# Performance work log

Measured on AMD Instinct MI355X. Metric: run time of the kernel, lower is better.

Reference implementation:

```python
import jax, jax.numpy as jnp
import numpy as np

N_USERS = 100000
N_LOCAS = 50000
N = N_USERS + N_LOCAS
D = 128   # embedding_dynamic_size
K = 128   # kg entity dim
S = 128   # static dim
NK = 50000  # kg rows
E = 2048  # number of events
LN_EPS = 1e-5
NORM_EPS = 1e-12


def setup_inputs() -> dict:
    key = jax.random.key(0)
    ks = jax.random.split(key, 24)
    f = jnp.float32
    rin = D + K + 1
    s_rnn = 1.0 / np.sqrt(D)
    s_pred = 1.0 / np.sqrt(2 * S + 2 * D + K)
    inp = {
        'embedding': jax.random.normal(ks[0], (N, D), f),
        'static': jax.random.normal(ks[1], (N, S), f),
        'kg': jax.random.normal(ks[2], (NK, K), f),
        'W_ih_u': jax.random.normal(ks[3], (D, rin), f) * s_rnn,
        'b_ih_u': jax.random.normal(ks[4], (D,), f) * s_rnn,
        'W_hh_u': jax.random.normal(ks[5], (D, D), f) * s_rnn,
        'b_hh_u': jax.random.normal(ks[6], (D,), f) * s_rnn,
        'W_ih_l': jax.random.normal(ks[7], (D, rin), f) * s_rnn,
        'b_ih_l': jax.random.normal(ks[8], (D,), f) * s_rnn,
        'W_hh_l': jax.random.normal(ks[9], (D, D), f) * s_rnn,
        'b_hh_l': jax.random.normal(ks[10], (D,), f) * s_rnn,
        'w_proj': jax.random.normal(ks[11], (D,), f),   # NormalLinear(1, D) weight, std=1/sqrt(1)=1
        'b_proj': jax.random.normal(ks[12], (D,), f),
        'ln_g': jnp.ones((D + K,), f),
        'ln_b': jnp.zeros((D + K,), f),
        'W_pred': jax.random.normal(ks[13], (S + D, 2 * S + 2 * D + K), f) * s_pred,
        'b_pred': jnp.zeros((S + D,), f),
        'delta_u': jax.random.uniform(ks[14], (E,), f),
        'delta_l': jax.random.uniform(ks[15], (E,), f),
        'idx_user': jax.random.randint(ks[16], (E,), 0, N_USERS, jnp.int32),
        'idx_loca': jax.random.randint(ks[17], (E,), 0, N_LOCAS, jnp.int32),
        'idx_prev': jax.random.randint(ks[18], (E,), 0, N_LOCAS, jnp.int32),
        'idx_know': jax.random.randint(ks[19], (E,), 0, NK, jnp.int32),
        'num_users': N_USERS,
    }
    return inp


def reference(embedding, static, kg, W_ih_u, b_ih_u, W_hh_u, b_hh_u,
              W_ih_l, b_ih_l, W_hh_l, b_hh_l, w_proj, b_proj, ln_g, ln_b,
              W_pred, b_pred, delta_u, delta_l,
              idx_user, idx_loca, idx_prev, idx_know, num_users):
    sg = jax.lax.stop_gradient

    def l2n(x):  # F.normalize along the feature dim (row vector)
        return x / jnp.maximum(jnp.linalg.norm(x), NORM_EPS)

    # event index preprocessing (matches idx_loca + num_users etc.)
    xs = (idx_user, idx_loca + num_users, idx_prev + num_users, idx_know,
          delta_u, delta_l)

    def step(carry, ev):
        emb, loss = carry
        iu, il, ip, ik, du, dl = ev
        u = emb[iu]        # [D]
        l = emb[il]        # [D]
        p = emb[ip]        # [D]
        kgr = kg[ik]       # [K]
        # projection: u * (1 + Linear(1->D)(delta_u))
        proj = u * (1.0 + w_proj * du + b_proj)
        # layer_norm over concat([emb_prev, kg_row]) of size D+K
        x = jnp.concatenate([p, kgr])
        mu = x.mean()
        var = jnp.mean((x - mu) ** 2)
        ln = (x - mu) / jnp.sqrt(var + LN_EPS) * ln_g + ln_b
        meta = jnp.concatenate([proj, ln, static[ip], static[iu]])  # [2S+2D+K]
        pred = W_pred @ meta + b_pred                               # [S+D]
        tgt = jnp.concatenate([l, static[il]])
        loss_pred = jnp.mean((pred - sg(tgt)) ** 2)
        # RNNCell updates (tanh), then L2-normalize
        x_u = jnp.concatenate([l, kgr, du[None]])
        new_u = l2n(jnp.tanh(W_ih_u @ x_u + b_ih_u + W_hh_u @ u + b_hh_u))
        x_l = jnp.concatenate([u, kgr, dl[None]])
        new_l = l2n(jnp.tanh(W_ih_l @ x_l + b_ih_l + W_hh_l @ l + b_hh_l))
        loss = loss + loss_pred \
                    + jnp.mean((new_u - sg(u)) ** 2) \
                    + jnp.mean((new_l - sg(l)) ** 2)
        emb = emb.at[iu].set(new_u).at[il].set(new_l)
        return (emb, loss), None

    (emb, loss), _ = jax.lax.scan(
        step, (embedding, jnp.asarray(0.0, embedding.dtype)), xs)
    return emb, loss
```

## Files before the change

### kernel.cpp

```cpp
#include <hip/hip_runtime.h>

#define DEVINL static __device__ __forceinline__

typedef float f32x4 __attribute__((ext_vector_type(4)));

constexpr int NUSER = 100000;
constexpr int D     = 128;
constexpr int METAN = 640;
constexpr int NT    = 256;
constexpr int CH    = 4;
constexpr int KP4   = 160;
constexpr int KR4   = 96;
constexpr int NCPY  = 1024;
constexpr int STW   = 640;

struct Params {
  const float *emb_in, *stat, *kg;
  const float *Wihu, *bihu, *Whhu, *bhhu;
  const float *Wihl, *bihl, *Whhl, *bhhl;
  const float *wproj, *bproj, *lng, *lnb, *Wpred, *bpred;
  const float *deltau, *deltal;
  const int *idxu, *idxl, *idxp, *idxk;
  float *emb;
  float *loss_slot;
  float *WpredT;
  float *WrnnT;
  float *brnn;
  float *wcol;
  float *loss_ev;
  float *stash;
  int *cnt_u, *cnt_w, *cnt_t;
  int *flag_u, *flag_l;
  int *done;
  int E, N, NLOC, NWORK;
};

DEVINL float loadx(const float* p) {
  return __hip_atomic_load(p, __ATOMIC_RELAXED, __HIP_MEMORY_SCOPE_AGENT);
}
DEVINL void storex(float* p, float v) {
  __hip_atomic_store(p, v, __ATOMIC_RELAXED, __HIP_MEMORY_SCOPE_AGENT);
}
DEVINL int loadcnt(const int* p) {
  return __hip_atomic_load(p, __ATOMIC_RELAXED, __HIP_MEMORY_SCOPE_AGENT);
}
DEVINL void storei(int* p, int v) {
  __hip_atomic_store(p, v, __ATOMIC_RELAXED, __HIP_MEMORY_SCOPE_AGENT);
}
DEVINL void sigadd(int* pp) {
  __hip_atomic_fetch_add(pp, 1, __ATOMIC_RELAXED, __HIP_MEMORY_SCOPE_AGENT);
}
DEVINL float dot4(float4 a, float4 b) { return a.x*b.x + a.y*b.y + a.z*b.z + a.w*b.w; }

DEVINL float4 block_sum4(float4 v, float4* s4) {
  #pragma unroll
  for (int o = 32; o; o >>= 1) {
    v.x += __shfl_xor(v.x, o, 64); v.y += __shfl_xor(v.y, o, 64);
    v.z += __shfl_xor(v.z, o, 64); v.w += __shfl_xor(v.w, o, 64);
  }
  if ((threadIdx.x & 63) == 0) s4[threadIdx.x >> 6] = v;
  __syncthreads();
  float4 r;
  r.x = s4[0].x + s4[1].x + s4[2].x + s4[3].x;
  r.y = s4[0].y + s4[1].y + s4[2].y + s4[3].y;
  r.z = s4[0].z + s4[1].z + s4[2].z + s4[3].z;
  r.w = s4[0].w + s4[1].w + s4[2].w + s4[3].w;
  __syncthreads();
  return r;
}

// ... 24 lines not shown
    float4 v = *(const float4*)(p.Wpred + (size_t)j * METAN + k4 * 4);
    ((float4*)p.WpredT)[k4 * 256 + j] = v;
  }
  for (int idx = tid; idx < 256 * KR4; idx += stride) {
    int j = idx / KR4, k4 = idx - j * KR4;
    int i = j & 127;
    const float* Wih = (j < 128) ? p.Wihu : p.Wihl;
    const float* Whh = (j < 128) ? p.Whhu : p.Whhl;
    float4 v; float* vp = (float*)&v;
    #pragma unroll
    for (int e = 0; e < 4; ++e) {
      int k = k4 * 4 + e;
      vp[e] = (k < 256) ? Wih[(size_t)i * 257 + k] : Whh[(size_t)i * 128 + (k - 256)];
    }
    ((float4*)p.WrnnT)[k4 * 256 + j] = v;
  }
  for (int j = tid; j < 256; j += stride) {
    int i = j & 127;
    p.brnn[j] = (j < 128) ? p.bihu[i] + p.bhhu[i] : p.bihl[i] + p.bhhl[i];
    p.wcol[j] = (j < 128) ? p.Wihu[(size_t)i * 257 + 256] : p.Wihl[(size_t)i * 257 + 256];
  }
}

__global__ __launch_bounds__(NT, 2) void k_main(Params p) {
  __shared__ __align__(16) float s_meta[CH][METAN];
  __shared__ __align__(16) float s_u[CH][D], s_l[CH][D], s_p[CH][D], s_kg[CH][D], s_sil[CH][D];
  __shared__ float4 s_r4[4];
  __shared__ unsigned long long s_redu[4][CH];
  __shared__ int s_ev[8][CH];
  __shared__ float s_dd[2][CH];

  const int tid = threadIdx.x, w = tid >> 6, lane = tid & 63;
  const int bid = blockIdx.x;

  if (bid >= p.NWORK && bid < p.NWORK + NCPY) {
    size_t gid = (size_t)(bid - p.NWORK) * NT + tid;
    size_t gs  = (size_t)NCPY * NT;
    size_t n4  = (size_t)p.N * 32;
    const f32x4* src = (const f32x4*)p.emb_in;
    f32x4* dst = (f32x4*)p.emb;
    size_t g = gid;
    for (; g + 3 * gs < n4; g += 4 * gs) {
      size_t g0 = g, g1 = g + gs, g2 = g + 2 * gs, g3 = g + 3 * gs;
      int r0 = (int)(g0 >> 5), r1 = (int)(g1 >> 5), r2 = (int)(g2 >> 5), r3 = (int)(g3 >> 5);
      int f0 = (r0 < NUSER) ? p.flag_u[r0] : p.flag_l[r0 - NUSER];
      int f1 = (r1 < NUSER) ? p.flag_u[r1] : p.flag_l[r1 - NUSER];
      int f2 = (r2 < NUSER) ? p.flag_u[r2] : p.flag_l[r2 - NUSER];
      int f3 = (r3 < NUSER) ? p.flag_u[r3] : p.flag_l[r3 - NUSER];
      f32x4 v0 = src[g0], v1 = src[g1], v2 = src[g2], v3 = src[g3];
      if (!f0) dst[g0] = v0;
      if (!f1) dst[g1] = v1;
      if (!f2) dst[g2] = v2;
      if (!f3) dst[g3] = v3;
    }
    for (; g < n4; g += gs) {
      int r = (int)(g >> 5);
      int f = (r < NUSER) ? p.flag_u[r] : p.flag_l[r - NUSER];
      f32x4 v = src[g];
      if (!f) dst[g] = v;
    }
    return;
  }

  const bool is_chain = (bid < p.NWORK);
  const int c = is_chain ? bid : bid - p.NWORK - NCPY;
  const int base = c * CH;
  const int nev = min(CH, p.E - base);
  if (nev <= 0) return;

  int iu_[CH], il_[CH], ip_[CH], ik_[CH];
  #pragma unroll
  for (int e = 0; e < CH; ++e) {
    int t = base + e; bool v = e < nev;
    iu_[e] = v ? p.idxu[t] : -1;
    il_[e] = v ? p.idxl[t] : -1;
    ip_[e] = v ? p.idxp[t] : -1;
    ik_[e] = v ? p.idxk[t] : 0;
  }

  if (is_chain) {
    float du_[CH], dl_[CH];
    #pragma unroll
    for (int e = 0; e < CH; ++e) {
      int t = base + e; bool v = e < nev;
      du_[e] = v ? p.deltau[t] : 0.f;
      dl_[e] = v ? p.deltal[t] : 0.f;
    }

    unsigned long long pk[CH] = {0ull,0ull,0ull,0ull};
    for (int s = tid; s < base; s += NT) {
      int ius = p.idxu[s], ils = p.idxl[s], ips = p.idxp[s];
      #pragma unroll
      for (int e = 0; e < CH; ++e) {
        unsigned long long a  = (ius == iu_[e]);
        unsigned long long wl = (ils == il_[e]);
        unsigned long long b  = (unsigned long long)((ils == il_[e]) + (ips == il_[e]));
        unsigned long long cc = (ils == ip_[e]);
        pk[e] += a | (wl << 16) | (b << 32) | (cc << 48);
      }
    }
    #pragma unroll
    for (int o = 32; o; o >>= 1) {
      #pragma unroll
      for (int e = 0; e < CH; ++e) pk[e] += __shfl_xor(pk[e], o, 64);
    }
    if (lane == 0) {
      #pragma unroll
      for (int e = 0; e < CH; ++e) s_redu[w][e] = pk[e];
    }
    __syncthreads();
    #pragma unroll
    for (int e = 0; e < CH; ++e)
      pk[e] = s_redu[0][e] + s_redu[1][e] + s_redu[2][e] + s_redu[3][e];
    __syncthreads();

    int A_[CH], WL_[CH], B_[CH], C_[CH];
    #pragma unroll
    for (int e = 0; e < CH; ++e) {
      int a  = (int)(pk[e] & 0xffff),        wl = (int)((pk[e] >> 16) & 0xffff);
      int b  = (int)((pk[e] >> 32) & 0xffff), cc = (int)((pk[e] >> 48) & 0xffff);
      #pragma unroll
      for (int s2 = 0; s2 < CH; ++s2) if (s2 < e) {
        a  += (iu_[s2] == iu_[e]);
        wl += (il_[s2] == il_[e]);
        b  += (il_[s2] == il_[e]) + (ip_[s2] == il_[e]);
        cc += (il_[s2] == ip_[e]);
      }
      A_[e] = a; WL_[e] = wl; B_[e] = b; C_[e] = cc;
    }
    bool internal = false;
    #pragma unroll
    for (int t2 = 1; t2 < CH; ++t2) if (t2 < nev) {
      #pragma unroll
      for (int s2 = 0; s2 < t2; ++s2)
        internal |= (iu_[s2] == iu_[t2]) | (il_[s2] == il_[t2]) |
                    (il_[s2] == ip_[t2]) | (ip_[s2] == il_[t2]);
    }

    if (tid == 0) {
      #pragma unroll
      for (int e = 0; e < CH; ++e) {
        s_ev[0][e] = iu_[e]; s_ev[1][e] = il_[e]; s_ev[2][e] = ip_[e];
        s_ev[3][e] = A_[e];  s_ev[4][e] = WL_[e]; s_ev[5][e] = B_[e];
        s_ev[6][e] = C_[e];  s_ev[7][e] = ik_[e];
        s_dd[0][e] = du_[e]; s_dd[1][e] = dl_[e];
      }
    }
    __syncthreads();

    auto PRELOAD = [&](int b0, int b1) {
      int e = w;
      if (e >= b0 && e < b1) {
        int iu = s_ev[0][e], ilr = s_ev[1][e] + NUSER, ipr = s_ev[2][e] + NUSER;
        int A = s_ev[3][e], WL = s_ev[4][e], Ck = s_ev[6][e], ik = s_ev[7][e];
        if (lane < 32) {
          int li = lane * 4;
          *(float4*)&s_kg[e][li] = *(const float4*)(p.kg + (size_t)ik * D + li);
        }
        int i0 = lane * 2;
        if (!A)  *(float2*)&s_u[e][i0] = *(const float2*)(p.emb_in + (size_t)iu  * D + i0);
        if (!WL) *(float2*)&s_l[e][i0] = *(const float2*)(p.emb_in + (size_t)ilr * D + i0);
        if (!Ck) *(float2*)&s_p[e][i0] = *(const float2*)(p.emb_in + (size_t)ipr * D + i0);
      }
    };

    auto SPIN = [&](int b0, int b1) {
      if (w == 0) {
        int e = b0 + lane;
        bool act = lane < (b1 - b0);
        int iu = 0, il = 0, ip = 0, A = 0, Bc = 0, Cc = 0;
        if (act) {
          iu = s_ev[0][e]; il = s_ev[1][e]; ip = s_ev[2][e];
          A = s_ev[3][e]; Bc = s_ev[5][e]; Cc = s_ev[6][e];
        }
        int guard = 0;
        while (true) {
          int x = loadcnt(&p.cnt_u[iu]);
          int y = loadcnt(&p.cnt_t[il]);
          int z = loadcnt(&p.cnt_w[ip]);
          bool ok = (!act) | ((x >= A) & (y >= Bc) & (z >= Cc));
          if (__all(ok)) break;
          if (++guard > (1 << 22)) break;
          __builtin_amdgcn_s_sleep(1);
        }
      }
      __syncthreads();
    };

    auto POSTLOAD = [&](int b0, int b1) {
      int e = w;
      if (e >= b0 && e < b1) {
        int iu = s_ev[0][e], ilr = s_ev[1][e] + NUSER, ipr = s_ev[2][e] + NUSER;
        int A = s_ev[3][e], WL = s_ev[4][e], Ck = s_ev[6][e];
        int i0 = lane * 2;
        if (A) {
          s_u[e][i0]   = loadx(p.emb + (size_t)iu * D + i0);
          s_u[e][i0+1] = loadx(p.emb + (size_t)iu * D + i0 + 1);
        }
        if (WL) {
          s_l[e][i0]   = loadx(p.emb + (size_t)ilr * D + i0);
          s_l[e][i0+1] = loadx(p.emb + (size_t)ilr * D + i0 + 1);
        }
        if (Ck) {
          s_p[e][i0]   = loadx(p.emb + (size_t)ipr * D + i0);
          s_p[e][i0+1] = loadx(p.emb + (size_t)ipr * D + i0 + 1);
        }
      }
    };

    auto RNNPROC = [&](int b0, int b1) {
      __syncthreads();
      const bool uc = (tid < 128);
      const float4* xo0 = (const float4*)(uc ? s_l[0] : s_u[0]);
      const float4* xo1 = (const float4*)(uc ? s_l[1] : s_u[1]);
      const float4* xo2 = (const float4*)(uc ? s_l[2] : s_u[2]);
      const float4* xo3 = (const float4*)(uc ? s_l[3] : s_u[3]);
      const float4* xk0 = (const float4*)s_kg[0];
      const float4* xk1 = (const float4*)s_kg[1];
      const float4* xk2 = (const float4*)s_kg[2];
      const float4* xk3 = (const float4*)s_kg[3];
      const float4* xs0 = (const float4*)(uc ? s_u[0] : s_l[0]);
      const float4* xs1 = (const float4*)(uc ? s_u[1] : s_l[1]);
      const float4* xs2 = (const float4*)(uc ? s_u[2] : s_l[2]);
      const float4* xs3 = (const float4*)(uc ? s_u[3] : s_l[3]);
      float ra0 = 0.f, ra1 = 0.f, ra2 = 0.f, ra3 = 0.f;
      const float4* wr = (const float4*)p.WrnnT + tid;
      #pragma unroll 8
      for (int k4 = 0; k4 < 32; ++k4) {
        float4 wv = wr[k4 * 256];
        ra0 += dot4(wv, xo0[k4]); ra1 += dot4(wv, xo1[k4]);
        ra2 += dot4(wv, xo2[k4]); ra3 += dot4(wv, xo3[k4]);
      }
      #pragma unroll 8
      for (int k4 = 32; k4 < 64; ++k4) {
        float4 wv = wr[k4 * 256];
        ra0 += dot4(wv, xk0[k4-32]); ra1 += dot4(wv, xk1[k4-32]);
        ra2 += dot4(wv, xk2[k4-32]); ra3 += dot4(wv, xk3[k4-32]);
      }
      #pragma unroll 8
      for (int k4 = 64; k4 < 96; ++k4) {
        float4 wv = wr[k4 * 256];
        ra0 += dot4(wv, xs0[k4-64]); ra1 += dot4(wv, xs1[k4-64]);
        ra2 += dot4(wv, xs2[k4-64]); ra3 += dot4(wv, xs3[k4-64]);
      }
      float brn = p.brnn[tid], wcv = p.wcol[tid];
      float d0 = uc ? s_dd[0][0] : s_dd[1][0];
      float d1 = uc ? s_dd[0][1] : s_dd[1][1];
      float d2 = uc ? s_dd[0][2] : s_dd[1][2];
      float d3 = uc ? s_dd[0][3] : s_dd[1][3];
      float h0 = tanhf(ra0 + brn + wcv * d0), h1 = tanhf(ra1 + brn + wcv * d1);
      float h2v = tanhf(ra2 + brn + wcv * d2), h3 = tanhf(ra3 + brn + wcv * d3);

      float4 SU, SL;
      half_sum4(make_float4(h0*h0, h1*h1, h2v*h2v, h3*h3), s_r4, &SU, &SL);
      float s0 = uc ? SU.x : SL.x, s1 = uc ? SU.y : SL.y;
      float s2 = uc ? SU.z : SL.z, s3 = uc ? SU.w : SL.w;
      float n0 = h0 / fmaxf(sqrtf(s0), 1e-12f), n1 = h1 / fmaxf(sqrtf(s1), 1e-12f);
      float n2 = h2v / fmaxf(sqrtf(s2), 1e-12f), n3 = h3 / fmaxf(sqrtf(s3), 1e-12f);

      float nv[CH] = {n0, n1, n2, n3};
      #pragma unroll
      for (int e = 0; e < CH; ++e) if (e >= b0 && e < b1) {
        if (tid < 128) storex(p.emb + (size_t)s_ev[0][e] * D + tid, nv[e]);
        else           storex(p.emb + ((size_t)s_ev[1][e] + NUSER) * D + (tid - 128), nv[e]);
      }
      __syncthreads();

      if (tid >= b0 && tid < b1) {
        __builtin_amdgcn_fence(__ATOMIC_RELEASE, "agent");
        sigadd(&p.cnt_u[s_ev[0][tid]]);
        sigadd(&p.cnt_t[s_ev[1][tid]]);
        sigadd(&p.cnt_w[s_ev[1][tid]]);
        sigadd(&p.cnt_t[s_ev[2][tid]]);
      }

      #pragma unroll
      for (int e = 0; e < CH; ++e) if (e >= b0 && e < b1) {
        float* st = p.stash + (size_t)(base + e) * STW;
        if (tid < 128) {
          storex(st + tid,       s_u[e][tid]);
          storex(st + 256 + tid, s_p[e][tid]);
          storex(st + 384 + tid, nv[e]);
        } else {
          int i = tid - 128;
          storex(st + 128 + i, s_l[e][i]);
          storex(st + 512 + i, nv[e]);
        }
      }
    };

    if (!internal) {
      PRELOAD(0, nev);
      SPIN(0, nev);
      POSTLOAD(0, nev);
      RNNPROC(0, nev);
    } else {
      for (int e = 0; e < nev; ++e) {
        PRELOAD(e, e + 1);
        SPIN(e, e + 1);
        POSTLOAD(e, e + 1);
        RNNPROC(e, e + 1);
      }
    }
    __syncthreads();
    if (tid == 0) storei(&p.done[c], 1);
    return;
  }

  {
    if (w == 0) {
      int guard = 0;
      while (!loadcnt(&p.done[c])) {
        if (++guard > (1 << 22)) break;
        __builtin_amdgcn_s_sleep(1);
      }
    }
    __syncthreads();

    if (w < nev) {
      int e = w;
      const float* st = p.stash + (size_t)(base + e) * STW;
      int iu = iu_[e], ilr = il_[e] + NUSER, ipr = ip_[e] + NUSER, ik = ik_[e];
      int i0 = lane * 2;
      s_u[e][i0]   = loadx(st + i0);
      s_u[e][i0+1] = loadx(st + i0 + 1);
      s_l[e][i0]   = loadx(st + 128 + i0);
      s_l[e][i0+1] = loadx(st + 128 + i0 + 1);
      s_p[e][i0]   = loadx(st + 256 + i0);
      s_p[e][i0+1] = loadx(st + 256 + i0 + 1);
      int h2 = lane >> 5, li = (lane & 31) * 4;
      if (h2 == 0) {
        *(float4*)&s_kg[e][li]         = *(const float4*)(p.kg   + (size_t)ik  * D + li);
        *(float4*)&s_meta[e][512 + li] = *(const float4*)(p.stat + (size_t)iu  * D + li);
      } else {
        *(float4*)&s_meta[e][384 + li] = *(const float4*)(p.stat + (size_t)ipr * D + li);
        *(float4*)&s_sil[e][li]        = *(const float4*)(p.stat + (size_t)ilr * D + li);
      }
    }
    __syncthreads();

    if (w < nev) {
      int e = w;
      float du = p.deltau[base + e];
      float4 xv = (lane < 32) ? *(const float4*)&s_p[e][lane * 4]
                              : *(const float4*)&s_kg[e][(lane - 32) * 4];
      float sm = xv.x + xv.y + xv.z + xv.w;
      #pragma unroll
      for (int o = 32; o; o >>= 1) sm += __shfl_xor(sm, o, 64);
      float mu = sm * (1.f / 256.f);
      float4 d = make_float4(xv.x - mu, xv.y - mu, xv.z - mu, xv.w - mu);
      float vs = d.x*d.x + d.y*d.y + d.z*d.z + d.w*d.w;
      #pragma unroll
      for (int o = 32; o; o >>= 1) vs += __shfl_xor(vs, o, 64);
      float rstd = rsqrtf(vs * (1.f / 256.f) + 1e-5f);
      int idx2 = lane * 4;
      float4 g  = *(const float4*)&p.lng[idx2];
      float4 bb = *(const float4*)&p.lnb[idx2];
      float4 lnv = make_float4(d.x*rstd*g.x + bb.x, d.y*rstd*g.y + bb.y,
                               d.z*rstd*g.z + bb.z, d.w*rstd*g.w + bb.w);
      if (lane < 32) *(float4*)&s_meta[e][128 + idx2] = lnv;
      else           *(float4*)&s_meta[e][128 + idx2] = lnv;
      int i0 = lane * 2;
      #pragma unroll
      for (int j = 0; j < 2; ++j) {
        int i = i0 + j;
        s_meta[e][i] = s_u[e][i] * (1.f + p.wproj[i] * du + p.bproj[i]);
      }
    }
    __syncthreads();

    const bool uc = (tid < 128);
    const float4* m40 = (const float4*)&s_meta[0][0];
    const float4* m41 = (const float4*)&s_meta[1][0];
    const float4* m42 = (const float4*)&s_meta[2][0];
    const float4* m43 = (const float4*)&s_meta[3][0];
    float pa0 = 0.f, pa1 = 0.f, pa2 = 0.f, pa3 = 0.f;
    const float4* wp = (const float4*)p.WpredT + tid;
    #pragma unroll 8
    for (int k4 = 0; k4 < KP4; ++k4) {
      float4 wv = wp[k4 * 256];
      pa0 += dot4(wv, m40[k4]); pa1 += dot4(wv, m41[k4]);
      pa2 += dot4(wv, m42[k4]); pa3 += dot4(wv, m43[k4]);
    }
    float bp = p.bpred[tid];
    float4 ep2;
    {
      float tg0 = uc ? s_l[0][tid] : s_sil[0][tid - 128];
      float tg1 = uc ? s_l[1][tid] : s_sil[1][tid - 128];
      float tg2 = uc ? s_l[2][tid] : s_sil[2][tid - 128];
      float tg3 = uc ? s_l[3][tid] : s_sil[3][tid - 128];
      float e0 = pa0 + bp - tg0, e1 = pa1 + bp - tg1;
      float e2 = pa2 + bp - tg2, e3 = pa3 + bp - tg3;
      ep2 = make_float4(e0*e0, e1*e1, e2*e2, e3*e3);
    }
    float4 LP = block_sum4(ep2, s_r4);

    const float* st0 = p.stash + (size_t)(base + 0) * STW;
    const float* st1 = p.stash + (size_t)(base + 1) * STW;
    const float* st2 = p.stash + (size_t)(base + 2) * STW;
    const float* st3 = p.stash + (size_t)(base + 3) * STW;
    int noff = uc ? (384 + tid) : (512 + tid - 128);
    float n0 = loadx(st0 + noff), n1 = loadx(st1 + noff);
    float n2 = loadx(st2 + noff), n3 = loadx(st3 + noff);
    float o0 = uc ? s_u[0][tid] : s_l[0][tid - 128];
    float o1 = uc ? s_u[1][tid] : s_l[1][tid - 128];
    float o2 = uc ? s_u[2][tid] : s_l[2][tid - 128];
    float o3 = uc ? s_u[3][tid] : s_l[3][tid - 128];
    float q0 = n0 - o0, q1 = n1 - o1, q2 = n2 - o2, q3 = n3 - o3;
    float4 LE = block_sum4(make_float4(q0*q0, q1*q1, q2*q2, q3*q3), s_r4);

    if (tid < nev) {
      float lp = (tid == 0) ? LP.x : (tid == 1) ? LP.y : (tid == 2) ? LP.z : LP.w;
      float le = (tid == 0) ? LE.x : (tid == 1) ? LE.y : (tid == 2) ? LE.z : LE.w;
      p.loss_ev[base + tid] = lp * (1.f / 256.f) + le * (1.f / 128.f);
    }
  }
}

__global__ void k_fin(Params p) {
  __shared__ float4 s_r4[4];
  float v = 0.f;
  for (int i = threadIdx.x; i < p.E; i += NT) v += p.loss_ev[i];
  float4 r = block_sum4(make_float4(v, 0.f, 0.f, 0.f), s_r4);
  if (threadIdx.x == 0) p.loss_slot[0] = r.x;
}

extern "C" void kernel_launch(void* const* d_in, const int* in_sizes, int n_in,
                              void* d_out, int out_size, void* d_ws, size_t ws_size,
                              hipStream_t stream) {
  Params p;
  p.emb_in = (const float*)d_in[0];
  p.stat   = (const float*)d_in[1];
  p.kg     = (const float*)d_in[2];
  p.Wihu = (const float*)d_in[3];   p.bihu = (const float*)d_in[4];
  p.Whhu = (const float*)d_in[5];   p.bhhu = (const float*)d_in[6];
  p.Wihl = (const float*)d_in[7];   p.bihl = (const float*)d_in[8];
  p.Whhl = (const float*)d_in[9];   p.bhhl = (const float*)d_in[10];
  p.wproj = (const float*)d_in[11]; p.bproj = (const float*)d_in[12];
// ... 13 lines not shown

  p.emb       = (float*)d_out;
  p.loss_slot = (float*)d_out + (size_t)p.N * D;

  char* ws = (char*)d_ws;
  size_t off = 0;
  auto take = [&](size_t bytes) {
    void* r = ws + off;
    off += (bytes + 255) & ~(size_t)255;
    return r;
  };
  p.WpredT  = (float*)take((size_t)KP4 * 256 * 16);
  p.WrnnT   = (float*)take((size_t)KR4 * 256 * 16);
  p.brnn    = (float*)take(256 * 4);
  p.wcol    = (float*)take(256 * 4);
  p.loss_ev = (float*)take((size_t)p.E * 4);
  p.stash   = (float*)take((size_t)p.E * STW * 4);
  size_t z0 = off;
  p.cnt_u   = (int*)take((size_t)NUSER * 4);
  p.cnt_w   = (int*)take((size_t)p.NLOC * 4);
  p.cnt_t   = (int*)take((size_t)p.NLOC * 4);
  p.flag_u  = (int*)take((size_t)NUSER * 4);
  p.flag_l  = (int*)take((size_t)p.NLOC * 4);
  p.done    = (int*)take((size_t)p.NWORK * 4);
  size_t zbytes = off - z0;

  hipMemsetAsync(ws + z0, 0, zbytes, stream);
  hipLaunchKernelGGL(k_init, dim3(512), dim3(NT), 0, stream, p);
  hipLaunchKernelGGL(k_main, dim3(p.NWORK * 2 + NCPY), dim3(NT), 0, stream, p);
  hipLaunchKernelGGL(k_fin,  dim3(1),   dim3(NT), 0, stream, p);
}
```

Before: 144.1 us.

## Split fused mega-kernel into separate chain, copy and loss kernels

```diff
diff --git a/kernel.cpp b/kernel.cpp
--- a/kernel.cpp
+++ b/kernel.cpp
@@ -11,7 +11,7 @@
 constexpr int CH    = 4;
 constexpr int KP4   = 160;
 constexpr int KR4   = 96;
-constexpr int NCPY  = 1024;
+constexpr int NCPY  = 2048;
 constexpr int STW   = 640;
 
 struct Params {
@@ -31,7 +31,6 @@
   float *stash;
   int *cnt_u, *cnt_w, *cnt_t;
   int *flag_u, *flag_l;
-  int *done;
   int E, N, NLOC, NWORK;
 };
 
@@ -43,9 +42,6 @@
 }
 DEVINL int loadcnt(const int* p) {
   return __hip_atomic_load(p, __ATOMIC_RELAXED, __HIP_MEMORY_SCOPE_AGENT);
-}
-DEVINL void storei(int* p, int v) {
-  __hip_atomic_store(p, v, __ATOMIC_RELAXED, __HIP_MEMORY_SCOPE_AGENT);
 }
 DEVINL void sigadd(int* pp) {
   __hip_atomic_fetch_add(pp, 1, __ATOMIC_RELAXED, __HIP_MEMORY_SCOPE_AGENT);
@@ -116,53 +112,49 @@
   }
 }
 
-__global__ __launch_bounds__(NT, 2) void k_main(Params p) {
-  __shared__ __align__(16) float s_meta[CH][METAN];
-  __shared__ __align__(16) float s_u[CH][D], s_l[CH][D], s_p[CH][D], s_kg[CH][D], s_sil[CH][D];
+__global__ __launch_bounds__(NT) void k_copy(Params p) {
+  size_t gid = (size_t)blockIdx.x * NT + threadIdx.x;
+  size_t gs  = (size_t)gridDim.x * NT;
+  size_t n4  = (size_t)p.N * 32;
+  const f32x4* src = (const f32x4*)p.emb_in;
+  f32x4* dst = (f32x4*)p.emb;
+  size_t g = gid;
+  for (; g + 3 * gs < n4; g += 4 * gs) {
+    size_t g0 = g, g1 = g + gs, g2 = g + 2 * gs, g3 = g + 3 * gs;
+    int r0 = (int)(g0 >> 5), r1 = (int)(g1 >> 5), r2 = (int)(g2 >> 5), r3 = (int)(g3 >> 5);
+    int f0 = (r0 < NUSER) ? p.flag_u[r0] : p.flag_l[r0 - NUSER];
+    int f1 = (r1 < NUSER) ? p.flag_u[r1] : p.flag_l[r1 - NUSER];
+    int f2 = (r2 < NUSER) ? p.flag_u[r2] : p.flag_l[r2 - NUSER];
+    int f3 = (r3 < NUSER) ? p.flag_u[r3] : p.flag_l[r3 - NUSER];
+    f32x4 v0 = src[g0], v1 = src[g1], v2 = src[g2], v3 = src[g3];
+    if (!f0) dst[g0] = v0;
+    if (!f1) dst[g1] = v1;
+    if (!f2) dst[g2] = v2;
+    if (!f3) dst[g3] = v3;
+  }
+  for (; g < n4; g += gs) {
+    int r = (int)(g >> 5);
+    int f = (r < NUSER) ? p.flag_u[r] : p.flag_l[r - NUSER];
+    f32x4 v = src[g];
+    if (!f) dst[g] = v;
+  }
+}
+
+__global__ __launch_bounds__(NT, 2) void k_chain(Params p) {
+  __shared__ __align__(16) float s_u[CH][D], s_l[CH][D], s_p[CH][D], s_kg[CH][D];
   __shared__ float4 s_r4[4];
   __shared__ unsigned long long s_redu[4][CH];
   __shared__ int s_ev[8][CH];
   __shared__ float s_dd[2][CH];
 
   const int tid = threadIdx.x, w = tid >> 6, lane = tid & 63;
-  const int bid = blockIdx.x;
-
-  if (bid >= p.NWORK && bid < p.NWORK + NCPY) {
-    size_t gid = (size_t)(bid - p.NWORK) * NT + tid;
-    size_t gs  = (size_t)NCPY * NT;
-    size_t n4  = (size_t)p.N * 32;
-    const f32x4* src = (const f32x4*)p.emb_in;
-    f32x4* dst = (f32x4*)p.emb;
-    size_t g = gid;
-    for (; g + 3 * gs < n4; g += 4 * gs) {
-      size_t g0 = g, g1 = g + gs, g2 = g + 2 * gs, g3 = g + 3 * gs;
-      int r0 = (int)(g0 >> 5), r1 = (int)(g1 >> 5), r2 = (int)(g2 >> 5), r3 = (int)(g3 >> 5);
-      int f0 = (r0 < NUSER) ? p.flag_u[r0] : p.flag_l[r0 - NUSER];
-      int f1 = (r1 < NUSER) ? p.flag_u[r1] : p.flag_l[r1 - NUSER];
-      int f2 = (r2 < NUSER) ? p.flag_u[r2] : p.flag_l[r2 - NUSER];
-      int f3 = (r3 < NUSER) ? p.flag_u[r3] : p.flag_l[r3 - NUSER];
-      f32x4 v0 = src[g0], v1 = src[g1], v2 = src[g2], v3 = src[g3];
-      if (!f0) dst[g0] = v0;
-      if (!f1) dst[g1] = v1;
-      if (!f2) dst[g2] = v2;
-      if (!f3) dst[g3] = v3;
-    }
-    for (; g < n4; g += gs) {
-      int r = (int)(g >> 5);
-      int f = (r < NUSER) ? p.flag_u[r] : p.flag_l[r - NUSER];
-      f32x4 v = src[g];
-      if (!f) dst[g] = v;
-    }
-    return;
-  }
-
-  const bool is_chain = (bid < p.NWORK);
-  const int c = is_chain ? bid : bid - p.NWORK - NCPY;
+  const int c = blockIdx.x;
   const int base = c * CH;
   const int nev = min(CH, p.E - base);
   if (nev <= 0) return;
 
   int iu_[CH], il_[CH], ip_[CH], ik_[CH];
+  float du_[CH], dl_[CH];
   #pragma unroll
   for (int e = 0; e < CH; ++e) {
     int t = base + e; bool v = e < nev;
@@ -170,344 +162,331 @@
     il_[e] = v ? p.idxl[t] : -1;
     ip_[e] = v ? p.idxp[t] : -1;
     ik_[e] = v ? p.idxk[t] : 0;
-  }
-
-  if (is_chain) {
-    float du_[CH], dl_[CH];
+    du_[e] = v ? p.deltau[t] : 0.f;
+    dl_[e] = v ? p.deltal[t] : 0.f;
+  }
+
+  unsigned long long pk[CH] = {0ull,0ull,0ull,0ull};
+  for (int s = tid; s < base; s += NT) {
+    int ius = p.idxu[s], ils = p.idxl[s], ips = p.idxp[s];
     #pragma unroll
     for (int e = 0; e < CH; ++e) {
-      int t = base + e; bool v = e < nev;
-      du_[e] = v ? p.deltau[t] : 0.f;
-      dl_[e] = v ? p.deltal[t] : 0.f;
-    }
-
-    unsigned long long pk[CH] = {0ull,0ull,0ull,0ull};
-    for (int s = tid; s < base; s += NT) {
-      int ius = p.idxu[s], ils = p.idxl[s], ips = p.idxp[s];
-      #pragma unroll
-      for (int e = 0; e < CH; ++e) {
-        unsigned long long a  = (ius == iu_[e]);
-        unsigned long long wl = (ils == il_[e]);
-        unsigned long long b  = (unsigned long long)((ils == il_[e]) + (ips == il_[e]));
-        unsigned long long cc = (ils == ip_[e]);
-        pk[e] += a | (wl << 16) | (b << 32) | (cc << 48);
-      }
-    }
-    #pragma unroll
-    for (int o = 32; o; o >>= 1) {
-      #pragma unroll
-      for (int e = 0; e < CH; ++e) pk[e] += __shfl_xor(pk[e], o, 64);
-    }
-    if (lane == 0) {
-      #pragma unroll
-      for (int e = 0; e < CH; ++e) s_redu[w][e] = pk[e];
-    }
-    __syncthreads();
-    #pragma unroll
-    for (int e = 0; e < CH; ++e)
-      pk[e] = s_redu[0][e] + s_redu[1][e] + s_redu[2][e] + s_redu[3][e];
-    __syncthreads();
-
-    int A_[CH], WL_[CH], B_[CH], C_[CH];
+      unsigned long long a  = (ius == iu_[e]);
+      unsigned long long wl = (ils == il_[e]);
+      unsigned long long b  = (unsigned long long)((ils == il_[e]) + (ips == il_[e]));
+      unsigned long long cc = (ils == ip_[e]);
+      pk[e] += a | (wl << 16) | (b << 32) | (cc << 48);
+    }
+  }
+  #pragma unroll
+  for (int o = 32; o; o >>= 1) {
+    #pragma unroll
+    for (int e = 0; e < CH; ++e) pk[e] += __shfl_xor(pk[e], o, 64);
+  }
+  if (lane == 0) {
+    #pragma unroll
+    for (int e = 0; e < CH; ++e) s_redu[w][e] = pk[e];
+  }
+  __syncthreads();
+  #pragma unroll
+  for (int e = 0; e < CH; ++e)
+    pk[e] = s_redu[0][e] + s_redu[1][e] + s_redu[2][e] + s_redu[3][e];
+  __syncthreads();
+
+  int A_[CH], WL_[CH], B_[CH], C_[CH];
+  #pragma unroll
+  for (int e = 0; e < CH; ++e) {
+    int a  = (int)(pk[e] & 0xffff),        wl = (int)((pk[e] >> 16) & 0xffff);
+    int b  = (int)((pk[e] >> 32) & 0xffff), cc = (int)((pk[e] >> 48) & 0xffff);
+    #pragma unroll
+    for (int s2 = 0; s2 < CH; ++s2) if (s2 < e) {
+      a  += (iu_[s2] == iu_[e]);
+      wl += (il_[s2] == il_[e]);
+      b  += (il_[s2] == il_[e]) + (ip_[s2] == il_[e]);
+      cc += (il_[s2] == ip_[e]);
+    }
+    A_[e] = a; WL_[e] = wl; B_[e] = b; C_[e] = cc;
+  }
+  bool internal = false;
+  #pragma unroll
+  for (int t2 = 1; t2 < CH; ++t2) if (t2 < nev) {
+    #pragma unroll
+    for (int s2 = 0; s2 < t2; ++s2)
+      internal |= (iu_[s2] == iu_[t2]) | (il_[s2] == il_[t2]) |
+                  (il_[s2] == ip_[t2]) | (ip_[s2] == il_[t2]);
+  }
+
+  if (tid == 0) {
     #pragma unroll
     for (int e = 0; e < CH; ++e) {
-      int a  = (int)(pk[e] & 0xffff),        wl = (int)((pk[e] >> 16) & 0xffff);
-      int b  = (int)((pk[e] >> 32) & 0xffff), cc = (int)((pk[e] >> 48) & 0xffff);
-      #pragma unroll
-      for (int s2 = 0; s2 < CH; ++s2) if (s2 < e) {
-        a  += (iu_[s2] == iu_[e]);
-        wl += (il_[s2] == il_[e]);
-        b  += (il_[s2] == il_[e]) + (ip_[s2] == il_[e]);
-        cc += (il_[s2] == ip_[e]);
-      }
-      A_[e] = a; WL_[e] = wl; B_[e] = b; C_[e] = cc;
-    }
-    bool internal = false;
-    #pragma unroll
-    for (int t2 = 1; t2 < CH; ++t2) if (t2 < nev) {
-      #pragma unroll
-      for (int s2 = 0; s2 < t2; ++s2)
-        internal |= (iu_[s2] == iu_[t2]) | (il_[s2] == il_[t2]) |
-                    (il_[s2] == ip_[t2]) | (ip_[s2] == il_[t2]);
-    }
-
-    if (tid == 0) {
-      #pragma unroll
-      for (int e = 0; e < CH; ++e) {
-        s_ev[0][e] = iu_[e]; s_ev[1][e] = il_[e]; s_ev[2][e] = ip_[e];
-        s_ev[3][e] = A_[e];  s_ev[4][e] = WL_[e]; s_ev[5][e] = B_[e];
-        s_ev[6][e] = C_[e];  s_ev[7][e] = ik_[e];
-        s_dd[0][e] = du_[e]; s_dd[1][e] = dl_[e];
-      }
-    }
-    __syncthreads();
-
-    auto PRELOAD = [&](int b0, int b1) {
-      int e = w;
-      if (e >= b0 && e < b1) {
-        int iu = s_ev[0][e], ilr = s_ev[1][e] + NUSER, ipr = s_ev[2][e] + NUSER;
-        int A = s_ev[3][e], WL = s_ev[4][e], Ck = s_ev[6][e], ik = s_ev[7][e];
-        if (lane < 32) {
-          int li = lane * 4;
-          *(float4*)&s_kg[e][li] = *(const float4*)(p.kg + (size_t)ik * D + li);
-        }
-        int i0 = lane * 2;
-        if (!A)  *(float2*)&s_u[e][i0] = *(const float2*)(p.emb_in + (size_t)iu  * D + i0);
-        if (!WL) *(float2*)&s_l[e][i0] = *(const float2*)(p.emb_in + (size_t)ilr * D + i0);
-        if (!Ck) *(float2*)&s_p[e][i0] = *(const float2*)(p.emb_in + (size_t)ipr * D + i0);
-      }
-    };
-
-    auto SPIN = [&](int b0, int b1) {
-      if (w == 0) {
-        int e = b0 + lane;
-        bool act = lane < (b1 - b0);
-        int iu = 0, il = 0, ip = 0, A = 0, Bc = 0, Cc = 0;
-        if (act) {
-          iu = s_ev[0][e]; il = s_ev[1][e]; ip = s_ev[2][e];
-          A = s_ev[3][e]; Bc = s_ev[5][e]; Cc = s_ev[6][e];
-        }
-        int guard = 0;
-        while (true) {
-          int x = loadcnt(&p.cnt_u[iu]);
-          int y = loadcnt(&p.cnt_t[il]);
-          int z = loadcnt(&p.cnt_w[ip]);
-          bool ok = (!act) | ((x >= A) & (y >= Bc) & (z >= Cc));
-          if (__all(ok)) break;
-          if (++guard > (1 << 22)) break;
-          __builtin_amdgcn_s_sleep(1);
-        }
-      }
-      __syncthreads();
-    };
-
-    auto POSTLOAD = [&](int b0, int b1) {
-      int e = w;
-      if (e >= b0 && e < b1) {
-        int iu = s_ev[0][e], ilr = s_ev[1][e] + NUSER, ipr = s_ev[2][e] + NUSER;
-        int A = s_ev[3][e], WL = s_ev[4][e], Ck = s_ev[6][e];
-        int i0 = lane * 2;
-        if (A) {
-          s_u[e][i0]   = loadx(p.emb + (size_t)iu * D + i0);
-          s_u[e][i0+1] = loadx(p.emb + (size_t)iu * D + i0 + 1);
-        }
-        if (WL) {
-          s_l[e][i0]   = loadx(p.emb + (size_t)ilr * D + i0);
-          s_l[e][i0+1] = loadx(p.emb + (size_t)ilr * D + i0 + 1);
-        }
-        if (Ck) {
-          s_p[e][i0]   = loadx(p.emb + (size_t)ipr * D + i0);
-          s_p[e][i0+1] = loadx(p.emb + (size_t)ipr * D + i0 + 1);
-        }
-      }
-    };
-
-    auto RNNPROC = [&](int b0, int b1) {
-      __syncthreads();
-      const bool uc = (tid < 128);
-      const float4* xo0 = (const float4*)(uc ? s_l[0] : s_u[0]);
-      const float4* xo1 = (const float4*)(uc ? s_l[1] : s_u[1]);
-      const float4* xo2 = (const float4*)(uc ? s_l[2] : s_u[2]);
-      const float4* xo3 = (const float4*)(uc ? s_l[3] : s_u[3]);
-      const float4* xk0 = (const float4*)s_kg[0];
-      const float4* xk1 = (const float4*)s_kg[1];
-      const float4* xk2 = (const float4*)s_kg[2];
-      const float4* xk3 = (const float4*)s_kg[3];
-      const float4* xs0 = (const float4*)(uc ? s_u[0] : s_l[0]);
-      const float4* xs1 = (const float4*)(uc ? s_u[1] : s_l[1]);
-      const float4* xs2 = (const float4*)(uc ? s_u[2] : s_l[2]);
-      const float4* xs3 = (const float4*)(uc ? s_u[3] : s_l[3]);
-      float ra0 = 0.f, ra1 = 0.f, ra2 = 0.f, ra3 = 0.f;
-      const float4* wr = (const float4*)p.WrnnT + tid;
-      #pragma unroll 8
-      for (int k4 = 0; k4 < 32; ++k4) {
-        float4 wv = wr[k4 * 256];
-        ra0 += dot4(wv, xo0[k4]); ra1 += dot4(wv, xo1[k4]);
-        ra2 += dot4(wv, xo2[k4]); ra3 += dot4(wv, xo3[k4]);
-      }
-      #pragma unroll 8
-      for (int k4 = 32; k4 < 64; ++k4) {
-        float4 wv = wr[k4 * 256];
-        ra0 += dot4(wv, xk0[k4-32]); ra1 += dot4(wv, xk1[k4-32]);
-        ra2 += dot4(wv, xk2[k4-32]); ra3 += dot4(wv, xk3[k4-32]);
-      }
-      #pragma unroll 8
-      for (int k4 = 64; k4 < 96; ++k4) {
-        float4 wv = wr[k4 * 256];
-        ra0 += dot4(wv, xs0[k4-64]); ra1 += dot4(wv, xs1[k4-64]);
-        ra2 += dot4(wv, xs2[k4-64]); ra3 += dot4(wv, xs3[k4-64]);
-      }
-      float brn = p.brnn[tid], wcv = p.wcol[tid];
-      float d0 = uc ? s_dd[0][0] : s_dd[1][0];
-      float d1 = uc ? s_dd[0][1] : s_dd[1][1];
-      float d2 = uc ? s_dd[0][2] : s_dd[1][2];
-      float d3 = uc ? s_dd[0][3] : s_dd[1][3];
-      float h0 = tanhf(ra0 + brn + wcv * d0), h1 = tanhf(ra1 + brn + wcv * d1);
-      float h2v = tanhf(ra2 + brn + wcv * d2), h3 = tanhf(ra3 + brn + wcv * d3);
-
-      float4 SU, SL;
-      half_sum4(make_float4(h0*h0, h1*h1, h2v*h2v, h3*h3), s_r4, &SU, &SL);
-      float s0 = uc ? SU.x : SL.x, s1 = uc ? SU.y : SL.y;
-      float s2 = uc ? SU.z : SL.z, s3 = uc ? SU.w : SL.w;
-      float n0 = h0 / fmaxf(sqrtf(s0), 1e-12f), n1 = h1 / fmaxf(sqrtf(s1), 1e-12f);
-      float n2 = h2v / fmaxf(sqrtf(s2), 1e-12f), n3 = h3 / fmaxf(sqrtf(s3), 1e-12f);
-
-      float nv[CH] = {n0, n1, n2, n3};
-      #pragma unroll
-      for (int e = 0; e < CH; ++e) if (e >= b0 && e < b1) {
-        if (tid < 128) storex(p.emb + (size_t)s_ev[0][e] * D + tid, nv[e]);
-        else           storex(p.emb + ((size_t)s_ev[1][e] + NUSER) * D + (tid - 128), nv[e]);
-      }
-      __syncthreads();
-
-      if (tid >= b0 && tid < b1) {
-        __builtin_amdgcn_fence(__ATOMIC_RELEASE, "agent");
-        sigadd(&p.cnt_u[s_ev[0][tid]]);
-        sigadd(&p.cnt_t[s_ev[1][tid]]);
-        sigadd(&p.cnt_w[s_ev[1][tid]]);
-        sigadd(&p.cnt_t[s_ev[2][tid]]);
-      }
-
-      #pragma unroll
-      for (int e = 0; e < CH; ++e) if (e >= b0 && e < b1) {
-        float* st = p.stash + (size_t)(base + e) * STW;
-        if (tid < 128) {
-          storex(st + tid,       s_u[e][tid]);
-          storex(st + 256 + tid, s_p[e][tid]);
-          storex(st + 384 + tid, nv[e]);
-        } else {
-          int i = tid - 128;
-          storex(st + 128 + i, s_l[e][i]);
-          storex(st + 512 + i, nv[e]);
-        }
-      }
-    };
-
-    if (!internal) {
-      PRELOAD(0, nev);
-      SPIN(0, nev);
-      POSTLOAD(0, nev);
-      RNNPROC(0, nev);
-    } else {
-      for (int e = 0; e < nev; ++e) {
-        PRELOAD(e, e + 1);
-        SPIN(e, e + 1);
-        POSTLOAD(e, e + 1);
-        RNNPROC(e, e + 1);
-      }
-    }
-    __syncthreads();
-    if (tid == 0) storei(&p.done[c], 1);
-    return;
-  }
-
-  {
+      s_ev[0][e] = iu_[e]; s_ev[1][e] = il_[e]; s_ev[2][e] = ip_[e];
+      s_ev[3][e] = A_[e];  s_ev[4][e] = WL_[e]; s_ev[5][e] = B_[e];
+      s_ev[6][e] = C_[e];  s_ev[7][e] = ik_[e];
+      s_dd[0][e] = du_[e]; s_dd[1][e] = dl_[e];
+    }
+  }
+  __syncthreads();
+
+  auto PRELOAD = [&](int b0, int b1) {
+    int e = w;
+    if (e >= b0 && e < b1) {
+      int iu = s_ev[0][e], ilr = s_ev[1][e] + NUSER, ipr = s_ev[2][e] + NUSER;
+      int A = s_ev[3][e], WL = s_ev[4][e], Ck = s_ev[6][e], ik = s_ev[7][e];
+      if (lane < 32) {
+        int li = lane * 4;
+        *(float4*)&s_kg[e][li] = *(const float4*)(p.kg + (size_t)ik * D + li);
+      }
+      int i0 = lane * 2;
+      if (!A)  *(float2*)&s_u[e][i0] = *(const float2*)(p.emb_in + (size_t)iu  * D + i0);
+      if (!WL) *(float2*)&s_l[e][i0] = *(const float2*)(p.emb_in + (size_t)ilr * D + i0);
+      if (!Ck) *(float2*)&s_p[e][i0] = *(const float2*)(p.emb_in + (size_t)ipr * D + i0);
+    }
+  };
+
+  auto SPIN = [&](int b0, int b1) {
     if (w == 0) {
+      int e = b0 + lane;
+      bool act = lane < (b1 - b0);
+      int iu = 0, il = 0, ip = 0, A = 0, Bc = 0, Cc = 0;
+      if (act) {
+        iu = s_ev[0][e]; il = s_ev[1][e]; ip = s_ev[2][e];
+        A = s_ev[3][e]; Bc = s_ev[5][e]; Cc = s_ev[6][e];
+      }
       int guard = 0;
-      while (!loadcnt(&p.done[c])) {
+      while (true) {
+        int x = loadcnt(&p.cnt_u[iu]);
+        int y = loadcnt(&p.cnt_t[il]);
+        int z = loadcnt(&p.cnt_w[ip]);
+        bool ok = (!act) | ((x >= A) & (y >= Bc) & (z >= Cc));
+        if (__all(ok)) break;
         if (++guard > (1 << 22)) break;
         __builtin_amdgcn_s_sleep(1);
       }
     }
     __syncthreads();
-
-    if (w < nev) {
-      int e = w;
-      const float* st = p.stash + (size_t)(base + e) * STW;
-      int iu = iu_[e], ilr = il_[e] + NUSER, ipr = ip_[e] + NUSER, ik = ik_[e];
+  };
+
+  auto POSTLOAD = [&](int b0, int b1) {
+    int e = w;
+    if (e >= b0 && e < b1) {
+      int iu = s_ev[0][e], ilr = s_ev[1][e] + NUSER, ipr = s_ev[2][e] + NUSER;
+      int A = s_ev[3][e], WL = s_ev[4][e], Ck = s_ev[6][e];
       int i0 = lane * 2;
-      s_u[e][i0]   = loadx(st + i0);
-      s_u[e][i0+1] = loadx(st + i0 + 1);
-      s_l[e][i0]   = loadx(st + 128 + i0);
-      s_l[e][i0+1] = loadx(st + 128 + i0 + 1);
-      s_p[e][i0]   = loadx(st + 256 + i0);
-      s_p[e][i0+1] = loadx(st + 256 + i0 + 1);
-      int h2 = lane >> 5, li = (lane & 31) * 4;
-      if (h2 == 0) {
-        *(float4*)&s_kg[e][li]         = *(const float4*)(p.kg   + (size_t)ik  * D + li);
-        *(float4*)&s_meta[e][512 + li] = *(const float4*)(p.stat + (size_t)iu  * D + li);
+      if (A) {
+        s_u[e][i0]   = loadx(p.emb + (size_t)iu * D + i0);
+        s_u[e][i0+1] = loadx(p.emb + (size_t)iu * D + i0 + 1);
+      }
+      if (WL) {
+        s_l[e][i0]   = loadx(p.emb + (size_t)ilr * D + i0);
+        s_l[e][i0+1] = loadx(p.emb + (size_t)ilr * D + i0 + 1);
+      }
+      if (Ck) {
+        s_p[e][i0]   = loadx(p.emb + (size_t)ipr * D + i0);
+        s_p[e][i0+1] = loadx(p.emb + (size_t)ipr * D + i0 + 1);
+      }
+    }
+  };
+
+  auto RNNPROC = [&](int b0, int b1) {
+    __syncthreads();
+    const bool uc = (tid < 128);
+    const float4* xo0 = (const float4*)(uc ? s_l[0] : s_u[0]);
+    const float4* xo1 = (const float4*)(uc ? s_l[1] : s_u[1]);
+    const float4* xo2 = (const float4*)(uc ? s_l[2] : s_u[2]);
+    const float4* xo3 = (const float4*)(uc ? s_l[3] : s_u[3]);
+    const float4* xk0 = (const float4*)s_kg[0];
+    const float4* xk1 = (const float4*)s_kg[1];
+    const float4* xk2 = (const float4*)s_kg[2];
+    const float4* xk3 = (const float4*)s_kg[3];
+    const float4* xs0 = (const float4*)(uc ? s_u[0] : s_l[0]);
+    const float4* xs1 = (const float4*)(uc ? s_u[1] : s_l[1]);
+    const float4* xs2 = (const float4*)(uc ? s_u[2] : s_l[2]);
+    const float4* xs3 = (const float4*)(uc ? s_u[3] : s_l[3]);
+    float ra0 = 0.f, ra1 = 0.f, ra2 = 0.f, ra3 = 0.f;
+    const float4* wr = (const float4*)p.WrnnT + tid;
+    #pragma unroll 8
+    for (int k4 = 0; k4 < 32; ++k4) {
+      float4 wv = wr[k4 * 256];
+      ra0 += dot4(wv, xo0[k4]); ra1 += dot4(wv, xo1[k4]);
+      ra2 += dot4(wv, xo2[k4]); ra3 += dot4(wv, xo3[k4]);
+    }
+    #pragma unroll 8
+    for (int k4 = 32; k4 < 64; ++k4) {
+      float4 wv = wr[k4 * 256];
+      ra0 += dot4(wv, xk0[k4-32]); ra1 += dot4(wv, xk1[k4-32]);
+      ra2 += dot4(wv, xk2[k4-32]); ra3 += dot4(wv, xk3[k4-32]);
+    }
+    #pragma unroll 8
+    for (int k4 = 64; k4 < 96; ++k4) {
+      float4 wv = wr[k4 * 256];
+      ra0 += dot4(wv, xs0[k4-64]); ra1 += dot4(wv, xs1[k4-64]);
+      ra2 += dot4(wv, xs2[k4-64]); ra3 += dot4(wv, xs3[k4-64]);
+    }
+    float brn = p.brnn[tid], wcv = p.wcol[tid];
+    float d0 = uc ? s_dd[0][0] : s_dd[1][0];
+    float d1 = uc ? s_dd[0][1] : s_dd[1][1];
+    float d2 = uc ? s_dd[0][2] : s_dd[1][2];
+    float d3 = uc ? s_dd[0][3] : s_dd[1][3];
+    float h0 = tanhf(ra0 + brn + wcv * d0), h1 = tanhf(ra1 + brn + wcv * d1);
+    float h2v = tanhf(ra2 + brn + wcv * d2), h3 = tanhf(ra3 + brn + wcv * d3);
+
+    float4 SU, SL;
+    half_sum4(make_float4(h0*h0, h1*h1, h2v*h2v, h3*h3), s_r4, &SU, &SL);
+    float s0 = uc ? SU.x : SL.x, s1 = uc ? SU.y : SL.y;
+    float s2 = uc ? SU.z : SL.z, s3 = uc ? SU.w : SL.w;
+    float n0 = h0 / fmaxf(sqrtf(s0), 1e-12f), n1 = h1 / fmaxf(sqrtf(s1), 1e-12f);
+    float n2 = h2v / fmaxf(sqrtf(s2), 1e-12f), n3 = h3 / fmaxf(sqrtf(s3), 1e-12f);
+
+    float nv[CH] = {n0, n1, n2, n3};
+    #pragma unroll
+    for (int e = 0; e < CH; ++e) if (e >= b0 && e < b1) {
+      if (tid < 128) storex(p.emb + (size_t)s_ev[0][e] * D + tid, nv[e]);
+      else           storex(p.emb + ((size_t)s_ev[1][e] + NUSER) * D + (tid - 128), nv[e]);
+    }
+    __syncthreads();
+
+    if (tid >= b0 && tid < b1) {
+      __builtin_amdgcn_fence(__ATOMIC_RELEASE, "agent");
+      sigadd(&p.cnt_u[s_ev[0][tid]]);
+      sigadd(&p.cnt_t[s_ev[1][tid]]);
+      sigadd(&p.cnt_w[s_ev[1][tid]]);
+      sigadd(&p.cnt_t[s_ev[2][tid]]);
+    }
+
+    #pragma unroll
+    for (int e = 0; e < CH; ++e) if (e >= b0 && e < b1) {
+      float* st = p.stash + (size_t)(base + e) * STW;
+      if (tid < 128) {
+        st[tid]       = s_u[e][tid];
+        st[256 + tid] = s_p[e][tid];
+        st[384 + tid] = nv[e];
       } else {
-        *(float4*)&s_meta[e][384 + li] = *(const float4*)(p.stat + (size_t)ipr * D + li);
-        *(float4*)&s_sil[e][li]        = *(const float4*)(p.stat + (size_t)ilr * D + li);
-      }
-    }
-    __syncthreads();
-
-    if (w < nev) {
-      int e = w;
-      float du = p.deltau[base + e];
-      float4 xv = (lane < 32) ? *(const float4*)&s_p[e][lane * 4]
-                              : *(const float4*)&s_kg[e][(lane - 32) * 4];
-      float sm = xv.x + xv.y + xv.z + xv.w;
-      #pragma unroll
-      for (int o = 32; o; o >>= 1) sm += __shfl_xor(sm, o, 64);
-      float mu = sm * (1.f / 256.f);
-      float4 d = make_float4(xv.x - mu, xv.y - mu, xv.z - mu, xv.w - mu);
-      float vs = d.x*d.x + d.y*d.y + d.z*d.z + d.w*d.w;
-      #pragma unroll
-      for (int o = 32; o; o >>= 1) vs += __shfl_xor(vs, o, 64);
-      float rstd = rsqrtf(vs * (1.f / 256.f) + 1e-5f);
-      int idx2 = lane * 4;
-      float4 g  = *(const float4*)&p.lng[idx2];
-      float4 bb = *(const float4*)&p.lnb[idx2];
-      float4 lnv = make_float4(d.x*rstd*g.x + bb.x, d.y*rstd*g.y + bb.y,
-                               d.z*rstd*g.z + bb.z, d.w*rstd*g.w + bb.w);
-      if (lane < 32) *(float4*)&s_meta[e][128 + idx2] = lnv;
-      else           *(float4*)&s_meta[e][128 + idx2] = lnv;
-      int i0 = lane * 2;
-      #pragma unroll
-      for (int j = 0; j < 2; ++j) {
-        int i = i0 + j;
-        s_meta[e][i] = s_u[e][i] * (1.f + p.wproj[i] * du + p.bproj[i]);
-      }
-    }
-    __syncthreads();
-
-    const bool uc = (tid < 128);
-    const float4* m40 = (const float4*)&s_meta[0][0];
-    const float4* m41 = (const float4*)&s_meta[1][0];
-    const float4* m42 = (const float4*)&s_meta[2][0];
-    const float4* m43 = (const float4*)&s_meta[3][0];
-    float pa0 = 0.f, pa1 = 0.f, pa2 = 0.f, pa3 = 0.f;
-    const float4* wp = (const float4*)p.WpredT + tid;
-    #pragma unroll 8
-    for (int k4 = 0; k4 < KP4; ++k4) {
-      float4 wv = wp[k4 * 256];
-      pa0 += dot4(wv, m40[k4]); pa1 += dot4(wv, m41[k4]);
-      pa2 += dot4(wv, m42[k4]); pa3 += dot4(wv, m43[k4]);
-    }
-    float bp = p.bpred[tid];
-    float4 ep2;
-    {
-      float tg0 = uc ? s_l[0][tid] : s_sil[0][tid - 128];
-      float tg1 = uc ? s_l[1][tid] : s_sil[1][tid - 128];
-      float tg2 = uc ? s_l[2][tid] : s_sil[2][tid - 128];
-      float tg3 = uc ? s_l[3][tid] : s_sil[3][tid - 128];
-      float e0 = pa0 + bp - tg0, e1 = pa1 + bp - tg1;
-      float e2 = pa2 + bp - tg2, e3 = pa3 + bp - tg3;
-      ep2 = make_float4(e0*e0, e1*e1, e2*e2, e3*e3);
-    }
-    float4 LP = block_sum4(ep2, s_r4);
-
-    const float* st0 = p.stash + (size_t)(base + 0) * STW;
-    const float* st1 = p.stash + (size_t)(base + 1) * STW;
-    const float* st2 = p.stash + (size_t)(base + 2) * STW;
-    const float* st3 = p.stash + (size_t)(base + 3) * STW;
-    int noff = uc ? (384 + tid) : (512 + tid - 128);
-    float n0 = loadx(st0 + noff), n1 = loadx(st1 + noff);
-    float n2 = loadx(st2 + noff), n3 = loadx(st3 + noff);
-    float o0 = uc ? s_u[0][tid] : s_l[0][tid - 128];
-    float o1 = uc ? s_u[1][tid] : s_l[1][tid - 128];
-    float o2 = uc ? s_u[2][tid] : s_l[2][tid - 128];
-    float o3 = uc ? s_u[3][tid] : s_l[3][tid - 128];
-    float q0 = n0 - o0, q1 = n1 - o1, q2 = n2 - o2, q3 = n3 - o3;
-    float4 LE = block_sum4(make_float4(q0*q0, q1*q1, q2*q2, q3*q3), s_r4);
-
-    if (tid < nev) {
-      float lp = (tid == 0) ? LP.x : (tid == 1) ? LP.y : (tid == 2) ? LP.z : LP.w;
-      float le = (tid == 0) ? LE.x : (tid == 1) ? LE.y : (tid == 2) ? LE.z : LE.w;
-      p.loss_ev[base + tid] = lp * (1.f / 256.f) + le * (1.f / 128.f);
-    }
+        int i = tid - 128;
+        st[128 + i] = s_l[e][i];
+        st[512 + i] = nv[e];
+      }
+    }
+  };
+
+  if (!internal) {
+    PRELOAD(0, nev);
+    SPIN(0, nev);
+    POSTLOAD(0, nev);
+    RNNPROC(0, nev);
+  } else {
+    for (int e = 0; e < nev; ++e) {
+      PRELOAD(e, e + 1);
+      SPIN(e, e + 1);
+      POSTLOAD(e, e + 1);
+      RNNPROC(e, e + 1);
+    }
+  }
+}
+
+__global__ __launch_bounds__(NT, 2) void k_loss(Params p) {
+  __shared__ __align__(16) float s_meta[CH][METAN];
+  __shared__ __align__(16) float s_u[CH][D], s_l[CH][D], s_p[CH][D], s_kg[CH][D], s_sil[CH][D];
+  __shared__ float4 s_r4[4];
+
+  const int tid = threadIdx.x, w = tid >> 6, lane = tid & 63;
+  const int c = blockIdx.x;
+  const int base = c * CH;
+  const int nev = min(CH, p.E - base);
+  if (nev <= 0) return;
+
+  if (w < nev) {
+    int e = w;
+    int t = base + e;
+    int iu = p.idxu[t], ilr = p.idxl[t] + NUSER, ipr = p.idxp[t] + NUSER, ik = p.idxk[t];
+    const float* st = p.stash + (size_t)t * STW;
+    int i0 = lane * 2;
+    *(float2*)&s_u[e][i0] = *(const float2*)(st + i0);
+    *(float2*)&s_l[e][i0] = *(const float2*)(st + 128 + i0);
+    *(float2*)&s_p[e][i0] = *(const float2*)(st + 256 + i0);
+    int h2 = lane >> 5, li = (lane & 31) * 4;
+    if (h2 == 0) {
+      *(float4*)&s_kg[e][li]         = *(const float4*)(p.kg   + (size_t)ik  * D + li);
+      *(float4*)&s_meta[e][512 + li] = *(const float4*)(p.stat + (size_t)iu  * D + li);
+    } else {
+      *(float4*)&s_meta[e][384 + li] = *(const float4*)(p.stat + (size_t)ipr * D + li);
+      *(float4*)&s_sil[e][li]        = *(const float4*)(p.stat + (size_t)ilr * D + li);
+    }
+  }
+  __syncthreads();
+
+  if (w < nev) {
+    int e = w;
+    float du = p.deltau[base + e];
+    float4 xv = (lane < 32) ? *(const float4*)&s_p[e][lane * 4]
+                            : *(const float4*)&s_kg[e][(lane - 32) * 4];
+    float sm = xv.x + xv.y + xv.z + xv.w;
+    #pragma unroll
+    for (int o = 32; o; o >>= 1) sm += __shfl_xor(sm, o, 64);
+    float mu = sm * (1.f / 256.f);
+    float4 d = make_float4(xv.x - mu, xv.y - mu, xv.z - mu, xv.w - mu);
+    float vs = d.x*d.x + d.y*d.y + d.z*d.z + d.w*d.w;
+    #pragma unroll
+    for (int o = 32; o; o >>= 1) vs += __shfl_xor(vs, o, 64);
+    float rstd = rsqrtf(vs * (1.f / 256.f) + 1e-5f);
+    int idx2 = lane * 4;
+    float4 g  = *(const float4*)&p.lng[idx2];
+    float4 bb = *(const float4*)&p.lnb[idx2];
+    *(float4*)&s_meta[e][128 + idx2] = make_float4(
+      d.x*rstd*g.x + bb.x, d.y*rstd*g.y + bb.y,
+      d.z*rstd*g.z + bb.z, d.w*rstd*g.w + bb.w);
+    int i0 = lane * 2;
+    #pragma unroll
+    for (int j = 0; j < 2; ++j) {
+      int i = i0 + j;
+      s_meta[e][i] = s_u[e][i] * (1.f + p.wproj[i] * du + p.bproj[i]);
+    }
+  }
+  __syncthreads();
+
+  const bool uc = (tid < 128);
+  const float4* m40 = (const float4*)&s_meta[0][0];
+  const float4* m41 = (const float4*)&s_meta[1][0];
+  const float4* m42 = (const float4*)&s_meta[2][0];
+  const float4* m43 = (const float4*)&s_meta[3][0];
+  float pa0 = 0.f, pa1 = 0.f, pa2 = 0.f, pa3 = 0.f;
+  const float4* wp = (const float4*)p.WpredT + tid;
+  #pragma unroll 8
+  for (int k4 = 0; k4 < KP4; ++k4) {
+    float4 wv = wp[k4 * 256];
+    pa0 += dot4(wv, m40[k4]); pa1 += dot4(wv, m41[k4]);
+    pa2 += dot4(wv, m42[k4]); pa3 += dot4(wv, m43[k4]);
+  }
+  float bp = p.bpred[tid];
+  float4 ep2;
+  {
+    float tg0 = uc ? s_l[0][tid] : s_sil[0][tid - 128];
+    float tg1 = uc ? s_l[1][tid] : s_sil[1][tid - 128];
+    float tg2 = uc ? s_l[2][tid] : s_sil[2][tid - 128];
+    float tg3 = uc ? s_l[3][tid] : s_sil[3][tid - 128];
+    float e0 = pa0 + bp - tg0, e1 = pa1 + bp - tg1;
+    float e2 = pa2 + bp - tg2, e3 = pa3 + bp - tg3;
+    ep2 = make_float4(e0*e0, e1*e1, e2*e2, e3*e3);
+  }
+  float4 LP = block_sum4(ep2, s_r4);
+
+  const float* st0 = p.stash + (size_t)(base + 0) * STW;
+  const float* st1 = p.stash + (size_t)(base + 1) * STW;
+  const float* st2 = p.stash + (size_t)(base + 2) * STW;
+  const float* st3 = p.stash + (size_t)(base + 3) * STW;
+  int noff = uc ? (384 + tid) : (512 + tid - 128);
+  float n0 = st0[noff], n1 = (nev > 1) ? st1[noff] : 0.f;
+  float n2 = (nev > 2) ? st2[noff] : 0.f, n3 = (nev > 3) ? st3[noff] : 0.f;
+  float o0 = uc ? s_u[0][tid] : s_l[0][tid - 128];
+  float o1 = uc ? s_u[1][tid] : s_l[1][tid - 128];
+  float o2 = uc ? s_u[2][tid] : s_l[2][tid - 128];
+  float o3 = uc ? s_u[3][tid] : s_l[3][tid - 128];
+  float q0 = n0 - o0, q1 = n1 - o1, q2 = n2 - o2, q3 = n3 - o3;
+  float4 LE = block_sum4(make_float4(q0*q0, q1*q1, q2*q2, q3*q3), s_r4);
+
+  if (tid < nev) {
+    float lp = (tid == 0) ? LP.x : (tid == 1) ? LP.y : (tid == 2) ? LP.z : LP.w;
+    float le = (tid == 0) ? LE.x : (tid == 1) ? LE.y : (tid == 2) ? LE.z : LE.w;
+    p.loss_ev[base + tid] = lp * (1.f / 256.f) + le * (1.f / 128.f);
   }
 }
 
@@ -567,11 +546,12 @@
   p.cnt_t   = (int*)take((size_t)p.NLOC * 4);
   p.flag_u  = (int*)take((size_t)NUSER * 4);
   p.flag_l  = (int*)take((size_t)p.NLOC * 4);
-  p.done    = (int*)take((size_t)p.NWORK * 4);
   size_t zbytes = off - z0;
 
   hipMemsetAsync(ws + z0, 0, zbytes, stream);
-  hipLaunchKernelGGL(k_init, dim3(512), dim3(NT), 0, stream, p);
-  hipLaunchKernelGGL(k_main, dim3(p.NWORK * 2 + NCPY), dim3(NT), 0, stream, p);
-  hipLaunchKernelGGL(k_fin,  dim3(1),   dim3(NT), 0, stream, p);
-}
+  hipLaunchKernelGGL(k_init,  dim3(512),     dim3(NT), 0, stream, p);
+  hipLaunchKernelGGL(k_chain, dim3(p.NWORK), dim3(NT), 0, stream, p);
+  hipLaunchKernelGGL(k_copy,  dim3(NCPY),    dim3(NT), 0, stream, p);
+  hipLaunchKernelGGL(k_loss,  dim3(p.NWORK), dim3(NT), 0, stream, p);
+  hipLaunchKernelGGL(k_fin,   dim3(1),       dim3(NT), 0, stream, p);
+}
```

Measured after the change: 178.2 us. +23.6%, slower.
